# Kernel tuning notes

Measured on AMD Instinct MI355X. Metric: run time of the kernel, lower is better.

Reference implementation:

```python
import jax, jax.numpy as jnp
import numpy as np

N_USER = 50000
N_ITEM = 50000
N_EDGE = 600000
D = 128


def _mean_agg(msg, dst, num_nodes):
    # segment-sum of messages and edge counts; nodes with no in-edges get 0 (DGL semantics)
    s = jax.ops.segment_sum(msg, dst, num_segments=num_nodes)
    cnt = jax.ops.segment_sum(jnp.ones((dst.shape[0], 1), msg.dtype), dst, num_segments=num_nodes)
    return s / jnp.maximum(cnt, 1.0)


def setup_inputs() -> dict:
    key = jax.random.key(0)
    ks = jax.random.split(key, 14)
    scale = 1.0 / np.sqrt(D)
    return {
        "feat_user": jax.random.normal(ks[0], (N_USER, D), jnp.float32),
        "feat_item": jax.random.normal(ks[1], (N_ITEM, D), jnp.float32),
        "W_uu": jax.random.normal(ks[2], (D, D), jnp.float32) * scale,
        "b_uu": jax.random.normal(ks[3], (D,), jnp.float32) * scale,
        "W_ub": jax.random.normal(ks[4], (D, D), jnp.float32) * scale,
        "b_ub": jax.random.normal(ks[5], (D,), jnp.float32) * scale,
        "W_iu": jax.random.normal(ks[6], (D, D), jnp.float32) * scale,
        "b_iu": jax.random.normal(ks[7], (D,), jnp.float32) * scale,
        "src_uu": jax.random.randint(ks[8], (N_EDGE,), 0, N_USER, jnp.int32),
        "dst_uu": jax.random.randint(ks[9], (N_EDGE,), 0, N_USER, jnp.int32),
        "src_ub": jax.random.randint(ks[10], (N_EDGE,), 0, N_USER, jnp.int32),
        "dst_ub": jax.random.randint(ks[11], (N_EDGE,), 0, N_ITEM, jnp.int32),
        "src_iu": jax.random.randint(ks[12], (N_EDGE,), 0, N_ITEM, jnp.int32),
        "dst_iu": jax.random.randint(ks[13], (N_EDGE,), 0, N_USER, jnp.int32),
    }


def reference(feat_user, feat_item, W_uu, b_uu, W_ub, b_ub, W_iu, b_iu,
              src_uu, dst_uu, src_ub, dst_ub, src_iu, dst_iu):
    # per-edge-type linear projection of src node features
    Wh_uu = feat_user @ W_uu + b_uu   # (user, follows, user)
    Wh_ub = feat_user @ W_ub + b_ub   # (user, buys, item)
    Wh_iu = feat_item @ W_iu + b_iu   # (item, bought_by, user)
    # copy_u -> mean per dst node, per edge type
    h_uu = _mean_agg(Wh_uu[src_uu], dst_uu, N_USER)
    h_ub = _mean_agg(Wh_ub[src_ub], dst_ub, N_ITEM)
    h_iu = _mean_agg(Wh_iu[src_iu], dst_iu, N_USER)
    # cross-type combine = 'sum' per dst ntype
    out_user = h_uu + h_iu
    out_item = h_ub
    return out_user, out_item
```

## Files before the change

### kernel.cpp

```cpp
#include <hip/hip_runtime.h>
#include <stdint.h>
#include <string.h>

#define N_USER 50000
#define N_ITEM 50000
#define N_EDGE 600000
#define D 128
#define NTOT 150000
#define ETOT 1800000
#define NB 147
#define BSH 10
#define SPAN 1024
#define CHUNK 4096

typedef unsigned short u16;
typedef unsigned int   u32;
typedef __attribute__((ext_vector_type(8))) short short8;
typedef __attribute__((ext_vector_type(4))) float floatx4;

static __device__ __forceinline__ u16 f2b(float f) {
  u32 x; memcpy(&x, &f, 4);
  u32 r = x + 0x7fffu + ((x >> 16) & 1u);
  return (u16)(r >> 16);
}
static __device__ __forceinline__ float blo2f(u32 v) {
  u32 x = v << 16; float f; memcpy(&f, &x, 4); return f;
}
static __device__ __forceinline__ float bhi2f(u32 v) {
  u32 x = v & 0xffff0000u; float f; memcpy(&f, &x, 4); return f;
}

__global__ void __launch_bounds__(256) k_front(
    const int* __restrict__ duu, const int* __restrict__ dub, const int* __restrict__ diu,
    int* __restrict__ bhist,
    const float* __restrict__ W0, const float* __restrict__ W1, const float* __restrict__ W2,
    u16* __restrict__ WT,
    const float* __restrict__ fu, const float* __restrict__ fi,
    u16* __restrict__ fb_u, u16* __restrict__ fb_i) {
  int bid = blockIdx.x;
  if (bid < 440) {
    __shared__ int h[NB];
    for (int i = threadIdx.x; i < NB; i += 256) h[i] = 0;
    __syncthreads();
    int base = bid * CHUNK;
    for (int j = threadIdx.x; j < CHUNK; j += 256) {
      int e = base + j;
      if (e < ETOT) {
        int t = e / N_EDGE, i = e - t * N_EDGE;
        int d = (t == 0) ? duu[i] : ((t == 1) ? dub[i] : diu[i]);
        atomicAdd(&h[(t * N_USER + d) >> BSH], 1);
      }
    }
    __syncthreads();
    for (int i = threadIdx.x; i < NB; i += 256) if (h[i]) atomicAdd(&bhist[i], h[i]);
  } else if (bid < 443) {
    int wsel = bid - 440;
    for (int idx = threadIdx.x; idx < D * D; idx += 256) {
      int n = idx >> 7, k = idx & 127;
      if (wsel == 0)      WT[n * 256 + k]       = f2b(W0[k * D + n]);
      else if (wsel == 1) WT[n * 256 + 128 + k] = f2b(W2[k * D + n]);
      else                WT[32768 + n * D + k] = f2b(W1[k * D + n]);
    }
  } else {
    int g = bid - 443;
    const float* src = fu; u16* dst = fb_u;
    if (g >= 6250) { g -= 6250; src = fi; dst = fb_i; }
    int gid = g * 256 + threadIdx.x;
    float4 v = ((const float4*)src)[gid];
    union { u16 u[4]; uint2 d; } pk;
    pk.u[0] = f2b(v.x); pk.u[1] = f2b(v.y); pk.u[2] = f2b(v.z); pk.u[3] = f2b(v.w);
    ((uint2*)dst)[gid] = pk.d;
  }
}

__global__ void __launch_bounds__(256) k_bplace(
    const int* __restrict__ suu, const int* __restrict__ duu,
    const int* __restrict__ sub, const int* __restrict__ dub,
    const int* __restrict__ siu, const int* __restrict__ diu,
    const int* __restrict__ bhist, int* __restrict__ cursor,
    int* __restrict__ boff, u32* __restrict__ ebuf) {
  __shared__ int h[NB];
  __shared__ int sboff[NB];
  __shared__ int buf[256];
  int t = threadIdx.x;
  int v = (t < NB) ? bhist[t] : 0;
  buf[t] = v; __syncthreads();
  for (int s = 1; s < 256; s <<= 1) {
    int y = (t >= s) ? buf[t - s] : 0;
    __syncthreads(); buf[t] += y; __syncthreads();
  }
  if (t < NB) sboff[t] = (t == 0) ? 0 : buf[t - 1];
  if (blockIdx.x == 0 && t <= NB) boff[t] = (t == 0) ? 0 : buf[t - 1];
  for (int i = t; i < NB; i += 256) h[i] = 0;
  __syncthreads();
  int base = blockIdx.x * CHUNK;
  u32 pay[16], br[16];
#pragma unroll
  for (int k = 0; k < 16; ++k) {
    int e = base + k * 256 + t;
    br[k] = 0xFFFFFFFFu;
    if (e < ETOT) {
      int ty = e / N_EDGE, i = e - ty * N_EDGE;
      int d, s;
      if (ty == 0)      { d = duu[i]; s = suu[i]; }
      else if (ty == 1) { d = dub[i]; s = sub[i]; }
      else              { d = diu[i]; s = siu[i]; }
      int slot = ty * N_USER + d;
      int bu = slot >> BSH;
      int rank = atomicAdd(&h[bu], 1);
      pay[k] = (u32)s | ((u32)(slot & (SPAN - 1)) << 16);
      br[k]  = (u32)bu | ((u32)rank << 8);
    }
  }
  __syncthreads();
  for (int i = t; i < NB; i += 256)
    h[i] = sboff[i] + atomicAdd(&cursor[i], h[i]);
  __syncthreads();
#pragma unroll
  for (int k = 0; k < 16; ++k) {
    if (br[k] != 0xFFFFFFFFu) {
      int bu = br[k] & 0xFF, rank = (int)(br[k] >> 8);
      ebuf[h[bu] + rank] = pay[k];
    }
  }
}

__global__ void __launch_bounds__(256) k_csr(const int* __restrict__ boff, const u32* __restrict__ ebuf,
                                             int* __restrict__ off, u16* __restrict__ ssrc) {
  __shared__ int sc[SPAN];
  __shared__ int so[SPAN];
  __shared__ int part[256];
  int b = blockIdx.x;
  int ebase = boff[b], ecnt = boff[b + 1] - ebase;
  int sbase = b << BSH;
  int nslots = (NTOT - sbase < SPAN) ? (NTOT - sbase) : SPAN;
  for (int i = threadIdx.x; i < SPAN; i += 256) sc[i] = 0;
  __syncthreads();
  for (int j = threadIdx.x; j < ecnt; j += 256)
    atomicAdd(&sc[ebuf[ebase + j] >> 16], 1);
  __syncthreads();
  int t = threadIdx.x;
  int s0 = sc[4*t], s1 = sc[4*t+1], s2 = sc[4*t+2], s3 = sc[4*t+3];
  int tsum = s0 + s1 + s2 + s3;
  part[t] = tsum; __syncthreads();
  for (int s = 1; s < 256; s <<= 1) {
    int y = (t >= s) ? part[t - s] : 0;
    __syncthreads(); part[t] += y; __syncthreads();
  }
  int pbase = part[t] - tsum;
  so[4*t]   = pbase;
  so[4*t+1] = pbase + s0;
  so[4*t+2] = pbase + s0 + s1;
  so[4*t+3] = pbase + s0 + s1 + s2;
  __syncthreads();
  for (int i = threadIdx.x; i < nslots; i += 256)
    off[sbase + i] = ebase + so[i];
  if (b == 0 && threadIdx.x == 0) off[NTOT] = ETOT;
  for (int i = threadIdx.x; i < SPAN; i += 256) sc[i] = so[i];
  __syncthreads();
  for (int j = threadIdx.x; j < ecnt; j += 256) {
    u32 p = ebuf[ebase + j];
    int pos = atomicAdd(&sc[p >> 16], 1);
    ssrc[ebase + pos] = (u16)(p & 0xFFFFu);
  }
}

__global__ void __launch_bounds__(256) k_mean(const u16* __restrict__ fb_u, const u16* __restrict__ fb_i,
                                              const int* __restrict__ off, const u16* __restrict__ ssrc,
                                              u16* __restrict__ ob) {
  int slot = blockIdx.x * 8 + (threadIdx.x >> 5);
  int lane = threadIdx.x & 31;
  if (slot >= NTOT) return;
  int t = slot / N_USER;
  int d = slot - t * N_USER;
  const u16* fb = (t == 2) ? fb_i : fb_u;
  int s = off[slot], e = off[slot + 1];
  int n = e - s;
  int my_src = (lane < n) ? (int)ssrc[s + lane] : 0;
  float a0 = 0.f, a1 = 0.f, a2 = 0.f, a3 = 0.f;
  int m = (n < 32) ? n : 32;
  int i = 0;
  for (; i + 4 <= m; i += 4) {
    int s0 = __shfl(my_src, i, 32);
    int s1 = __shfl(my_src, i + 1, 32);
    int s2 = __shfl(my_src, i + 2, 32);
    int s3 = __shfl(my_src, i + 3, 32);
    uint2 v0 = ((const uint2*)(fb + (size_t)s0 * D))[lane];
    uint2 v1 = ((const uint2*)(fb + (size_t)s1 * D))[lane];
    uint2 v2 = ((const uint2*)(fb + (size_t)s2 * D))[lane];
    uint2 v3 = ((const uint2*)(fb + (size_t)s3 * D))[lane];
    a0 += blo2f(v0.x) + blo2f(v1.x) + blo2f(v2.x) + blo2f(v3.x);
    a1 += bhi2f(v0.x) + bhi2f(v1.x) + bhi2f(v2.x) + bhi2f(v3.x);
    a2 += blo2f(v0.y) + blo2f(v1.y) + blo2f(v2.y) + blo2f(v3.y);
    a3 += bhi2f(v0.y) + bhi2f(v1.y) + bhi2f(v2.y) + bhi2f(v3.y);
  }
  for (; i < m; ++i) {
    int sr = __shfl(my_src, i, 32);
    uint2 v = ((const uint2*)(fb + (size_t)sr * D))[lane];
    a0 += blo2f(v.x); a1 += bhi2f(v.x);
    a2 += blo2f(v.y); a3 += bhi2f(v.y);
  }
  for (int j = s + 32; j < e; ++j) {
    int sr = ssrc[j];
    uint2 v = ((const uint2*)(fb + (size_t)sr * D))[lane];
    a0 += blo2f(v.x); a1 += bhi2f(v.x);
    a2 += blo2f(v.y); a3 += bhi2f(v.y);
  }
  float inv = (n > 0) ? 1.0f / (float)n : 0.f;
  u32 p0 = (u32)f2b(a0 * inv) | ((u32)f2b(a1 * inv) << 16);
  u32 p1 = (u32)f2b(a2 * inv) | ((u32)f2b(a3 * inv) << 16);
  u32* mrow;
  if (t == 0)      mrow = (u32*)(ob + (size_t)d * 256);
  else if (t == 2) mrow = (u32*)(ob + (size_t)d * 256 + 128);
  else             mrow = (u32*)(ob + 12800000 + (size_t)d * 256);
  ((uint2*)mrow)[lane] = make_uint2(p0, p1);
}

__global__ void __launch_bounds__(256, 4) k_out(float* out, const u16* __restrict__ WT,
                                                const float* __restrict__ buu, const float* __restrict__ bub,
                                                const float* __restrict__ biu, const int* __restrict__ off) {
  int users = (blockIdx.y == 0);
  int tid = threadIdx.x;
  int w = tid >> 6, lane = tid & 63, quad = lane >> 4, l16 = lane & 15;
  int row_base = blockIdx.x * 64 + w * 16;
  int r0 = row_base + l16;
  int rA = r0 < N_USER ? r0 : N_USER - 1;
  const u16* ob = (const u16*)out;

  floatx4 acc[8];
#pragma unroll
  for (int i = 0; i < 8; i++) acc[i] = (floatx4){0.f, 0.f, 0.f, 0.f};

  if (users) {
    const u16* A = ob + (size_t)rA * 256 + quad * 8;
    const u16* B = WT + l16 * 256 + quad * 8;
#pragma unroll
    for (int kk = 0; kk < 8; ++kk) {
      short8 af = *(const short8*)(A + kk * 32);
      short8 bf[8];
#pragma unroll
      for (int nt = 0; nt < 8; ++nt)
        bf[nt] = *(const short8*)(B + nt * 4096 + kk * 32);
#pragma unroll
      for (int nt = 0; nt < 8; ++nt)
        acc[nt] = __builtin_amdgcn_mfma_f32_16x16x32_bf16(af, bf[nt], acc[nt], 0, 0, 0);
    }
  } else {
    const u16* A = ob + 12800000 + (size_t)rA * 256 + quad * 8;
    const u16* B = WT + 32768 + l16 * 128 + quad * 8;
#pragma unroll
    for (int kk = 0; kk < 4; ++kk) {
      short8 af = *(const short8*)(A + kk * 32);
      short8 bf[8];
#pragma unroll
      for (int nt = 0; nt < 8; ++nt)
        bf[nt] = *(const short8*)(B + nt * 2048 + kk * 32);
#pragma unroll
      for (int nt = 0; nt < 8; ++nt)
        acc[nt] = __builtin_amdgcn_mfma_f32_16x16x32_bf16(af, bf[nt], acc[nt], 0, 0, 0);
    }
  }

  int nA[4], nB[4];
#pragma unroll
  for (int i = 0; i < 4; ++i) {
    int grow = row_base + quad * 4 + i;
    bool ok = grow < N_USER;
    if (users) {
      nA[i] = ok ? (off[grow + 1] - off[grow]) : 0;
      nB[i] = ok ? (off[2 * N_USER + grow + 1] - off[2 * N_USER + grow]) : 0;
    } else {
      nA[i] = ok ? (off[N_USER + grow + 1] - off[N_USER + grow]) : 0;
      nB[i] = 0;
    }
  }

#pragma unroll
  for (int nt = 0; nt < 8; ++nt) {
    int col = nt * 16 + l16;
    float bA = users ? buu[col] : bub[col];
    float bB = users ? biu[col] : 0.f;
#pragma unroll
    for (int i = 0; i < 4; ++i) {
      int grow = row_base + quad * 4 + i;
      if (grow < N_USER) {
        float r = acc[nt][i] + (nA[i] > 0 ? bA : 0.f) + (nB[i] > 0 ? bB : 0.f);
        out[(size_t)(users ? grow : N_USER + grow) * D + col] = r;
      }
    }
  }
}

extern "C" void kernel_launch(void* const* d_in, const int* in_sizes, int n_in,
                              void* d_out, int out_size, void* d_ws, size_t ws_size,
                              hipStream_t stream) {
  const float* fu  = (const float*)d_in[0];
  const float* fi  = (const float*)d_in[1];
  const float* Wuu = (const float*)d_in[2];
  const float* buu = (const float*)d_in[3];
  const float* Wub = (const float*)d_in[4];
  const float* bub = (const float*)d_in[5];
  const float* Wiu = (const float*)d_in[6];
  const float* biu = (const float*)d_in[7];
  const int* suu = (const int*)d_in[8];
  const int* duu = (const int*)d_in[9];
  const int* sub = (const int*)d_in[10];
  const int* dub = (const int*)d_in[11];
  const int* siu = (const int*)d_in[12];
  const int* diu = (const int*)d_in[13];
  float* out = (float*)d_out;
  u16* ob = (u16*)d_out;

  int* wsi    = (int*)d_ws;
  int* off    = wsi;
  int* bhist  = wsi + 150016;
  int* cursor = wsi + 150208;
  int* boff   = wsi + 150400;
  u32* ebuf   = (u32*)(wsi + 150592);
  u16* ssrc   = (u16*)(wsi + 1950592);
  u16* WT     = (u16*)(wsi + 2850592);
  u16* fb_u   = (u16*)(wsi + 2875168);
  u16* fb_i   = (u16*)(wsi + 6075168);

  hipMemsetAsync(bhist, 0, 384 * sizeof(int), stream);
  k_front<<<443 + 12500, 256, 0, stream>>>(duu, dub, diu, bhist, Wuu, Wub, Wiu, WT,
                                           fu, fi, fb_u, fb_i);
  k_bplace<<<440, 256, 0, stream>>>(suu, duu, sub, dub, siu, diu, bhist, cursor, boff, ebuf);
  k_csr<<<NB, 256, 0, stream>>>(boff, ebuf, off, ssrc);
  k_mean<<<18750, 256, 0, stream>>>(fb_u, fb_i, off, ssrc, ob);
  k_out<<<dim3(782, 2), 256, 0, stream>>>(out, WT, buu, bub, biu, off);
}
```

Before: 303.8 us.

## Stage projection weights in LDS and compute two row tiles per wave

The output GEMM kernel now copies the bf16 weight fragments for its edge type into a 64KB shared-memory buffer, already arranged in MFMA fragment order. Each wave then computes 32 rows instead of 16, so every weight fragment it reads from shared memory feeds two MFMAs. The grid is halved and launch bounds drop to 2 blocks per CU. This removes repeated per-wave global or L2 reads of the weights. In exchange, every block pays an up-front staging copy and a barrier, and the large shared allocation limits occupancy.

```diff
diff --git a/kernel.cpp b/kernel.cpp
--- a/kernel.cpp
+++ b/kernel.cpp
@@ -216,76 +216,83 @@
   ((uint2*)mrow)[lane] = make_uint2(p0, p1);
 }
 
-__global__ void __launch_bounds__(256, 4) k_out(float* out, const u16* __restrict__ WT,
+__global__ void __launch_bounds__(256, 2) k_out(float* out, const u16* __restrict__ WT,
                                                 const float* __restrict__ buu, const float* __restrict__ bub,
                                                 const float* __restrict__ biu, const int* __restrict__ off) {
   int users = (blockIdx.y == 0);
   int tid = threadIdx.x;
   int w = tid >> 6, lane = tid & 63, quad = lane >> 4, l16 = lane & 15;
-  int row_base = blockIdx.x * 64 + w * 16;
-  int r0 = row_base + l16;
-  int rA = r0 < N_USER ? r0 : N_USER - 1;
+  int KT = users ? 8 : 4;
+  const u16* Wsrc = users ? WT : (WT + 32768);
+  int wstride = users ? 256 : 128;
+
+  __shared__ u16 sB[32768];
+  int nfrag = KT * 8 * 64;
+  for (int fid = tid; fid < nfrag; fid += 256) {
+    int fl = fid & 63, fnt = (fid >> 6) & 7, fkk = fid >> 9;
+    int fq = fl >> 4, fl16 = fl & 15;
+    const u16* src = Wsrc + (fnt * 16 + fl16) * wstride + fkk * 32 + fq * 8;
+    *(uint4*)(sB + (size_t)fid * 8) = *(const uint4*)src;
+  }
+  __syncthreads();
+
+  int row0 = blockIdx.x * 128 + w * 32;
   const u16* ob = (const u16*)out;
-
-  floatx4 acc[8];
-#pragma unroll
-  for (int i = 0; i < 8; i++) acc[i] = (floatx4){0.f, 0.f, 0.f, 0.f};
-
-  if (users) {
-    const u16* A = ob + (size_t)rA * 256 + quad * 8;
-    const u16* B = WT + l16 * 256 + quad * 8;
-#pragma unroll
-    for (int kk = 0; kk < 8; ++kk) {
-      short8 af = *(const short8*)(A + kk * 32);
-      short8 bf[8];
-#pragma unroll
-      for (int nt = 0; nt < 8; ++nt)
-        bf[nt] = *(const short8*)(B + nt * 4096 + kk * 32);
-#pragma unroll
-      for (int nt = 0; nt < 8; ++nt)
-        acc[nt] = __builtin_amdgcn_mfma_f32_16x16x32_bf16(af, bf[nt], acc[nt], 0, 0, 0);
-    }
-  } else {
-    const u16* A = ob + 12800000 + (size_t)rA * 256 + quad * 8;
-    const u16* B = WT + 32768 + l16 * 128 + quad * 8;
-#pragma unroll
-    for (int kk = 0; kk < 4; ++kk) {
-      short8 af = *(const short8*)(A + kk * 32);
-      short8 bf[8];
-#pragma unroll
-      for (int nt = 0; nt < 8; ++nt)
-        bf[nt] = *(const short8*)(B + nt * 2048 + kk * 32);
-#pragma unroll
-      for (int nt = 0; nt < 8; ++nt)
-        acc[nt] = __builtin_amdgcn_mfma_f32_16x16x32_bf16(af, bf[nt], acc[nt], 0, 0, 0);
-    }
-  }
-
-  int nA[4], nB[4];
-#pragma unroll
-  for (int i = 0; i < 4; ++i) {
-    int grow = row_base + quad * 4 + i;
-    bool ok = grow < N_USER;
-    if (users) {
-      nA[i] = ok ? (off[grow + 1] - off[grow]) : 0;
-      nB[i] = ok ? (off[2 * N_USER + grow + 1] - off[2 * N_USER + grow]) : 0;
-    } else {
-      nA[i] = ok ? (off[N_USER + grow + 1] - off[N_USER + grow]) : 0;
-      nB[i] = 0;
-    }
-  }
-
-#pragma unroll
-  for (int nt = 0; nt < 8; ++nt) {
-    int col = nt * 16 + l16;
-    float bA = users ? buu[col] : bub[col];
-    float bB = users ? biu[col] : 0.f;
+  const u16* Abase = users ? ob : (ob + 12800000);
+  size_t outoff = users ? 0 : (size_t)N_USER;
+
+  int r0a = row0 + l16, r1a = row0 + 16 + l16;
+  int rA0 = r0a < N_USER ? r0a : N_USER - 1;
+  int rA1 = r1a < N_USER ? r1a : N_USER - 1;
+  const u16* A0 = Abase + (size_t)rA0 * 256 + quad * 8;
+  const u16* A1 = Abase + (size_t)rA1 * 256 + quad * 8;
+
+  floatx4 acc[2][8];
+#pragma unroll
+  for (int rt = 0; rt < 2; ++rt)
+#pragma unroll
+    for (int nt = 0; nt < 8; ++nt) acc[rt][nt] = (floatx4){0.f, 0.f, 0.f, 0.f};
+
+  for (int kk = 0; kk < KT; ++kk) {
+    short8 af0 = *(const short8*)(A0 + kk * 32);
+    short8 af1 = *(const short8*)(A1 + kk * 32);
+    const short8* bp = (const short8*)(sB + ((size_t)kk * 8 * 64 + lane) * 8);
+#pragma unroll
+    for (int nt = 0; nt < 8; ++nt) {
+      short8 bf = bp[nt * 64];
+      acc[0][nt] = __builtin_amdgcn_mfma_f32_16x16x32_bf16(af0, bf, acc[0][nt], 0, 0, 0);
+      acc[1][nt] = __builtin_amdgcn_mfma_f32_16x16x32_bf16(af1, bf, acc[1][nt], 0, 0, 0);
+    }
+  }
+
+#pragma unroll
+  for (int rt = 0; rt < 2; ++rt) {
+    int tbase = row0 + rt * 16;
+    int nA[4], nB[4];
 #pragma unroll
     for (int i = 0; i < 4; ++i) {
-      int grow = row_base + quad * 4 + i;
-      if (grow < N_USER) {
-        float r = acc[nt][i] + (nA[i] > 0 ? bA : 0.f) + (nB[i] > 0 ? bB : 0.f);
-        out[(size_t)(users ? grow : N_USER + grow) * D + col] = r;
+      int grow = tbase + quad * 4 + i;
+      bool ok = grow < N_USER;
+      if (users) {
+        nA[i] = ok ? (off[grow + 1] - off[grow]) : 0;
+        nB[i] = ok ? (off[2 * N_USER + grow + 1] - off[2 * N_USER + grow]) : 0;
+      } else {
+        nA[i] = ok ? (off[N_USER + grow + 1] - off[N_USER + grow]) : 0;
+        nB[i] = 0;
+      }
+    }
+#pragma unroll
+    for (int nt = 0; nt < 8; ++nt) {
+      int col = nt * 16 + l16;
+      float bA = users ? buu[col] : bub[col];
+      float bB = users ? biu[col] : 0.f;
+#pragma unroll
+      for (int i = 0; i < 4; ++i) {
+        int grow = tbase + quad * 4 + i;
+        if (grow < N_USER) {
+          float r = acc[rt][nt][i] + (nA[i] > 0 ? bA : 0.f) + (nB[i] > 0 ? bB : 0.f);
+          out[(outoff + (size_t)grow) * D + col] = r;
+        }
       }
     }
   }
@@ -328,5 +335,5 @@
   k_bplace<<<440, 256, 0, stream>>>(suu, duu, sub, dub, siu, diu, bhist, cursor, boff, ebuf);
   k_csr<<<NB, 256, 0, stream>>>(boff, ebuf, off, ssrc);
   k_mean<<<18750, 256, 0, stream>>>(fb_u, fb_i, off, ssrc, ob);
-  k_out<<<dim3(782, 2), 256, 0, stream>>>(out, WT, buu, bub, biu, off);
-}
+  k_out<<<dim3(391, 2), 256, 0, stream>>>(out, WT, buu, bub, biu, off);
+}
```

After: 286.4 us. 5.7% less time.
